# Optimization experiments

Hardware: AMD Instinct MI355X
Metric: run time of the kernel (lower is better)

The kernel has to match this reference:

```python
import jax, jax.numpy as jnp
import numpy as np

B, T, I, H, L = 128, 256, 512, 1024, 2


def setup_inputs() -> dict:
    key = jax.random.key(0)
    ks = jax.random.split(key, 9)
    s_i = 1.0 / np.sqrt(H)
    inp = {
        "x": jax.random.normal(ks[0], (B, T, I), dtype=jnp.float32),
        # layer 0: input_size -> hidden_size
        "W_ih0": jax.random.uniform(ks[1], (4 * H, I), dtype=jnp.float32, minval=-s_i, maxval=s_i),
        "W_hh0": jax.random.uniform(ks[2], (4 * H, H), dtype=jnp.float32, minval=-s_i, maxval=s_i),
        "b_ih0": jax.random.uniform(ks[3], (4 * H,), dtype=jnp.float32, minval=-s_i, maxval=s_i),
        "b_hh0": jax.random.uniform(ks[4], (4 * H,), dtype=jnp.float32, minval=-s_i, maxval=s_i),
        # layer 1: hidden_size -> hidden_size
        "W_ih1": jax.random.uniform(ks[5], (4 * H, H), dtype=jnp.float32, minval=-s_i, maxval=s_i),
        "W_hh1": jax.random.uniform(ks[6], (4 * H, H), dtype=jnp.float32, minval=-s_i, maxval=s_i),
        "b_ih1": jax.random.uniform(ks[7], (4 * H,), dtype=jnp.float32, minval=-s_i, maxval=s_i),
        "b_hh1": jax.random.uniform(ks[8], (4 * H,), dtype=jnp.float32, minval=-s_i, maxval=s_i),
    }
    return inp


def _lstm_cell(xt, h, c, W_ih, W_hh, b_ih, b_hh):
    # gates: [B, 4H] in order i, f, g, o (standard LSTMCell layout)
    gates = xt @ W_ih.T + b_ih + h @ W_hh.T + b_hh
    i, f, g, o = jnp.split(gates, 4, axis=-1)
    c_new = jax.nn.sigmoid(f) * c + jax.nn.sigmoid(i) * jnp.tanh(g)
    h_new = jax.nn.sigmoid(o) * jnp.tanh(c_new)
    return h_new, c_new


def reference(x, W_ih0, W_hh0, b_ih0, b_hh0, W_ih1, W_hh1, b_ih1, b_hh1):
    batch = x.shape[0]
    hidden = W_hh0.shape[1]
    params = ((W_ih0, W_hh0, b_ih0, b_hh0), (W_ih1, W_hh1, b_ih1, b_hh1))
    z = jnp.zeros((batch, hidden), dtype=x.dtype)
    # torch code initializes h and c both from h0 (zeros)
    init = (tuple(z for _ in params), tuple(z for _ in params))

    def step(carry, xt):
        hs, cs = carry
        new_h, new_c = [], []
        layer_in = xt
        for l, (Wi, Wh, bi, bh) in enumerate(params):
            h2, c2 = _lstm_cell(layer_in, hs[l], cs[l], Wi, Wh, bi, bh)
            new_h.append(h2)
            new_c.append(c2)
            layer_in = h2
        return (tuple(new_h), tuple(new_c)), layer_in

    xs = jnp.swapaxes(x, 0, 1)  # [T, B, I]
    _, ys = jax.lax.scan(step, init, xs)
    out = jnp.swapaxes(ys, 0, 1)  # [B, T, H]
    return out
```

## Files before the change

### kernel.cpp

```cpp
#include <hip/hip_runtime.h>

#define B_ 128
#define T_ 256
#define I_ 512
#define H_ 1024

typedef _Float16 f16;
typedef _Float16 v8h __attribute__((ext_vector_type(8)));
typedef _Float16 v2h __attribute__((ext_vector_type(2)));
typedef float v16f __attribute__((ext_vector_type(16)));
typedef int v4i __attribute__((ext_vector_type(4)));

__device__ __forceinline__ float fsigmoid(float x) { return 1.0f / (1.0f + __expf(-x)); }
__device__ __forceinline__ float ftanh(float x) { return 1.0f - 2.0f / (__expf(2.0f * x) + 1.0f); }

__device__ __forceinline__ void gl_lds16(const void* g, void* l) {
    __builtin_amdgcn_global_load_lds(
        (const __attribute__((address_space(1))) unsigned int*)g,
        (__attribute__((address_space(3))) unsigned int*)l, 16, 0, 0);
}
__device__ __forceinline__ void gl_lds16_coh(const void* g, void* l) {
    __builtin_amdgcn_global_load_lds(
        (const __attribute__((address_space(1))) unsigned int*)g,
        (__attribute__((address_space(3))) unsigned int*)l, 16, 0, 17);
}

__device__ __forceinline__ void pollwait(const int* base, int tgt, int lane) {
    if (tgt <= 0) return;
    for (;;) {
        bool ok = true;
        if (lane < 32) {
            v4i v;
            asm volatile("global_load_dwordx4 %0, %1, off sc0 sc1\n\ts_waitcnt vmcnt(0)"
                         : "=&v"(v) : "v"(base + lane * 4) : "memory");
            ok = (v[0] >= tgt) && (v[1] >= tgt) && (v[2] >= tgt) && (v[3] >= tgt);
        }
        if (__ballot(ok) == ~0ULL) return;
        __builtin_amdgcn_s_sleep(1);
    }
}

#define WAITV(n) asm volatile("s_waitcnt vmcnt(" #n ")" ::: "memory")
#define BARX { __builtin_amdgcn_s_barrier(); __builtin_amdgcn_sched_barrier(0); }

__global__ void k_f32_to_f16(const float* __restrict__ in, f16* __restrict__ out, int n) {
    int i = blockIdx.x * blockDim.x + threadIdx.x;
    int st = gridDim.x * blockDim.x;
    for (; i < n; i += st) out[i] = (f16)in[i];
}
__global__ void k_bias_sum(const float* __restrict__ a, const float* __restrict__ b,
                           float* __restrict__ o, int n) {
    int i = blockIdx.x * blockDim.x + threadIdx.x;
    int st = gridDim.x * blockDim.x;
    for (; i < n; i += st) o[i] = a[i] + b[i];
}

template <int SLOT>
__device__ void run_slot8(int mh, int tile, int widx128,
                          const f16* __restrict__ xh,
                          const f16* __restrict__ wi, const f16* __restrict__ wh,
                          const float* __restrict__ bs,
                          f16* __restrict__ h0, f16* __restrict__ h1,
                          float* __restrict__ out, int* flags, char* lds)
{
    constexpr int NKS = SLOT ? 32 : 24;
    const size_t BH = (size_t)B_ * H_;

    const int tid = threadIdx.x;
    const int wave = tid >> 6;
    const int lane = tid & 63;
    const int l31 = lane & 31, khi = lane >> 5;
    const int nw = wave & 1, kw = wave >> 1;
    const int n0 = tile * 16;
    const int rbase = mh * 64;

    const int gcl = nw * 32 + l31;
    const size_t gr = (size_t)(gcl >> 4) * H_ + n0 + (gcl & 15);
    v8h wfrag[NKS];
#pragma unroll
    for (int s = 0; s < NKS; ++s) {
        const f16* p;
        if (SLOT == 0) {
            p = (s < 8) ? (wi + gr * 512 + kw * 128 + s * 16 + khi * 8)
                        : (wh + gr * 1024 + kw * 256 + (s - 8) * 16 + khi * 8);
        } else {
            p = (s < 16) ? (wh + gr * 1024 + kw * 256 + s * 16 + khi * 8)
                         : (wi + gr * 1024 + kw * 256 + (s - 16) * 16 + khi * 8);
        }
        wfrag[s] = *(const v8h*)p;
    }

    const int urow = tid >> 3;
    const int un = (tid & 7) * 2;
    const float2 bI = *(const float2*)(bs + 0 * H_ + n0 + un);
    const float2 bF = *(const float2*)(bs + 1 * H_ + n0 + un);
    const float2 bG = *(const float2*)(bs + 2 * H_ + n0 + un);
    const float2 bO = *(const float2*)(bs + 3 * H_ + n0 + un);
    float c0r = 0.f, c1r = 0.f;

    int* f_own = flags + SLOT * 128;
    int* f_oth = flags + (1 - SLOT) * 128;

    float* gf = (float*)(lds + 49152);

    const int rw_ = lane >> 3;
    const int ss_ = (lane & 7) ^ rw_;

#pragma unroll 1
    for (int p = 0; p <= T_; ++p) {
        const bool active = SLOT ? (p >= 1) : (p < T_);
        const int tau = SLOT ? p - 1 : p;

        const f16* srcA = nullptr; size_t strA = 0; const f16* srcB = nullptr; f16* hout = nullptr;
        if (active) {
            if (SLOT == 0) {
                srcA = xh + (size_t)tau * I_;  strA = (size_t)T_ * I_;
                srcB = h0 + (size_t)((p + 3) & 3) * BH;
                hout = h0 + (size_t)(p & 3) * BH;
            } else {
                srcA = h0 + (size_t)((p + 3) & 3) * BH;
                srcB = h1 + (size_t)((p + 3) & 3) * BH;
                hout = h1 + (size_t)(p & 3) * BH;
            }
        }

        auto issue = [&](int r) {
            const f16* base; size_t str; int koff; bool coh;
            if (SLOT == 0) {
                if (r < 2) { base = srcA; str = strA;      koff = kw * 128 + r * 64;       coh = false; }
                else       { base = srcB; str = (size_t)H_; koff = kw * 256 + (r - 2) * 64; coh = true; }
            } else {
                if (r < 4) { base = srcB; str = (size_t)H_; koff = kw * 256 + r * 64;       coh = true; }
                else       { base = srcA; str = (size_t)H_; koff = kw * 256 + (r - 4) * 64; coh = true; }
            }
            char* dbase = lds + kw * 32768 + (r & 3) * 8192 + nw * 4096;
#pragma unroll
            for (int i = 0; i < 4; ++i) {
                const int rl = rbase + nw * 32 + i * 8 + rw_;
                const f16* gp = base + (size_t)rl * str + koff + ss_ * 8;
                if (coh) gl_lds16_coh(gp, dbase + i * 1024);
                else     gl_lds16(gp, dbase + i * 1024);
            }
        };

        v16f acc0 = {}, acc1 = {};

        auto compute = [&](int r) {
            const char* sb = lds + kw * 32768 + (r & 3) * 8192;
#pragma unroll
            for (int ks = 0; ks < 4; ++ks) {
                const int qo = (((ks * 2 + khi) ^ (l31 & 7)) << 4);
                const v8h a0 = *(const v8h*)(sb + l31 * 128 + qo);
                const v8h a1 = *(const v8h*)(sb + (32 + l31) * 128 + qo);
                __builtin_amdgcn_s_setprio(1);
                acc0 = __builtin_amdgcn_mfma_f32_32x32x16_f16(a0, wfrag[r * 4 + ks], acc0, 0, 0, 0);
                acc1 = __builtin_amdgcn_mfma_f32_32x32x16_f16(a1, wfrag[r * 4 + ks], acc1, 0, 0, 0);
                __builtin_amdgcn_s_setprio(0);
            }
        };

        if (active) {
            if (SLOT == 0) {
                issue(0); issue(1);
                WAITV(4); BARX; compute(0);
                WAITV(0); BARX; compute(1);
                if (wave == 0) pollwait(f_own, p, lane);
                BARX;
                issue(2); issue(3); issue(4);
                WAITV(8); BARX; compute(2); issue(5);
                WAITV(8); BARX; compute(3);
                WAITV(4); BARX; compute(4);
                WAITV(0); BARX; compute(5);
            } else {
                if (wave == 4) pollwait(f_own, p, lane);
                __syncthreads();
                issue(0); issue(1); issue(2);
                WAITV(8); BARX; compute(0); issue(3);
                WAITV(8); BARX; compute(1);
                if (wave == 0) pollwait(f_oth, p, lane);
                BARX;
                issue(4);
                WAITV(8); BARX; compute(2); issue(5);
                WAITV(8); BARX; compute(3); issue(6);
                WAITV(8); BARX; compute(4); issue(7);
                WAITV(8); BARX; compute(5);
                WAITV(4); BARX; compute(6);
                WAITV(0); BARX; compute(7);
            }
            __syncthreads();

            if (kw >= 1) {
                float* rg = (float*)lds + ((kw - 1) * 2 + nw) * 2048;
#pragma unroll
                for (int j = 0; j < 16; ++j) {
                    rg[j * 64 + lane] = acc0[j];
                    rg[(16 + j) * 64 + lane] = acc1[j];
                }
            }
            __syncthreads();
            if (kw == 0) {
                const float* r0 = (float*)lds + (0 + nw) * 2048;
                const float* r1 = (float*)lds + (2 + nw) * 2048;
                const float* r2 = (float*)lds + (4 + nw) * 2048;
#pragma unroll
                for (int j = 0; j < 16; ++j) {
                    const float s0 = acc0[j] + r0[j * 64 + lane] + r1[j * 64 + lane] + r2[j * 64 + lane];
                    const float s1 = acc1[j] + r0[(16 + j) * 64 + lane] + r1[(16 + j) * 64 + lane] + r2[(16 + j) * 64 + lane];
                    const int row = (j & 3) + 8 * (j >> 2) + 4 * khi;
                    gf[row * 68 + nw * 32 + l31] = s0;
                    gf[(32 + row) * 68 + nw * 32 + l31] = s1;
                }
            }
            __syncthreads();

            if (SLOT == 0) {
                if (wave == 0) pollwait(f_oth, p - 2, lane);
                __syncthreads();
            }

            {
                const float* g0 = gf + urow * 68 + un;
                const float xi0 = g0[0] + bI.x,  xi1 = g0[1] + bI.y;
                const float xf0 = g0[16] + bF.x, xf1 = g0[17] + bF.y;
                const float xg0 = g0[32] + bG.x, xg1 = g0[33] + bG.y;
                const float xo0 = g0[48] + bO.x, xo1 = g0[49] + bO.y;
                const float cn0 = fsigmoid(xf0) * c0r + fsigmoid(xi0) * ftanh(xg0);
                const float cn1 = fsigmoid(xf1) * c1r + fsigmoid(xi1) * ftanh(xg1);
                const float hn0 = fsigmoid(xo0) * ftanh(cn0);
                const float hn1 = fsigmoid(xo1) * ftanh(cn1);
                c0r = cn0; c1r = cn1;
                union { v2h h2; unsigned u; } cv;
                cv.h2[0] = (f16)hn0; cv.h2[1] = (f16)hn1;
                unsigned* hp = (unsigned*)(hout + (size_t)(rbase + urow) * H_ + n0 + un);
                asm volatile("global_store_dword %0, %1, off sc0 sc1" :: "v"(hp), "v"(cv.u) : "memory");
                if (SLOT == 1) {
                    float2 yv; yv.x = hn0; yv.y = hn1;
                    *(float2*)(out + ((size_t)(rbase + urow) * T_ + tau) * H_ + n0 + un) = yv;
                }
            }
        }

        asm volatile("s_waitcnt vmcnt(0)" ::: "memory");
        __syncthreads();
        if (tid == 0) {
            int v = p + 1;
            int* fp = f_own + widx128;
            asm volatile("global_store_dword %0, %1, off sc0 sc1" :: "v"(fp), "v"(v) : "memory");
        }
    }
}

__global__ __launch_bounds__(512, 2) void lstm_persist8(
    const f16* __restrict__ xh,
    const f16* __restrict__ w0i, const f16* __restrict__ w0h,
    const f16* __restrict__ w1i, const f16* __restrict__ w1h,
    const float* __restrict__ bs0, const float* __restrict__ bs1,
    f16* __restrict__ h0, f16* __restrict__ h1, float* __restrict__ out,
    int* flags)
{
    __shared__ __align__(16) char lds[131072];
    const int bx = blockIdx.x;
    const int slot = bx & 1;
    const int mh = (bx >> 1) & 1;
    const int tile = bx >> 2;
    const int widx128 = mh * 64 + tile;
    if (slot == 0)
        run_slot8<0>(mh, tile, widx128, xh, w0i, w0h, bs0, h0, h1, out, flags, lds);
    else
        run_slot8<1>(mh, tile, widx128, xh, w1i, w1h, bs1, h0, h1, out, flags, lds);
}

#define BM 64
#define NT 8

__global__ __launch_bounds__(256) void lstm_step(
    const float* __restrict__ A1, long a1_stride, int K1,
    const float* __restrict__ hprev,
    const float* __restrict__ Wih, const float* __restrict__ Whh,
    const float* __restrict__ bih, const float* __restrict__ bhh,
    float* __restrict__ cbuf, float* __restrict__ hout,
    float* yout, long y_stride)
{
    __shared__ float As[32][66];
    __shared__ float Ws[32][36];
    const int tid = threadIdx.x;
    const int n0 = blockIdx.x * NT;
    const int b0 = blockIdx.y * BM;
    const int tb = tid >> 3;
    const int tc = tid & 7;
    const int lr = tid >> 3;
    const int lk = tid & 7;
    const long wj = (long)(lr >> 3) * H_ + n0 + (lr & 7);
    float acc[2][4] = {{0.f, 0.f, 0.f, 0.f}, {0.f, 0.f, 0.f, 0.f}};
#pragma unroll 1
    for (int ph = 0; ph < 2; ++ph) {
        const float* Ap = (ph == 0) ? A1 : hprev;
        const long as = (ph == 0) ? a1_stride : (long)H_;
        const float* W = (ph == 0) ? Wih : Whh;
        const int K = (ph == 0) ? K1 : H_;
        const float* arow0 = Ap + (long)(b0 + lr) * as + 4 * lk;
        const float* arow1 = Ap + (long)(b0 + lr + 32) * as + 4 * lk;
        const float* wrow = W + wj * K + 4 * lk;
        float4 ra0 = *(const float4*)(arow0);
        float4 ra1 = *(const float4*)(arow1);
        float4 rw = *(const float4*)(wrow);
        for (int k0 = 0; k0 < K; k0 += 32) {
            __syncthreads();
            {
                const int kk = 4 * lk;
                As[kk + 0][lr] = ra0.x; As[kk + 1][lr] = ra0.y;
                As[kk + 2][lr] = ra0.z; As[kk + 3][lr] = ra0.w;
                As[kk + 0][lr + 32] = ra1.x; As[kk + 1][lr + 32] = ra1.y;
                As[kk + 2][lr + 32] = ra1.z; As[kk + 3][lr + 32] = ra1.w;
                Ws[kk + 0][lr] = rw.x; Ws[kk + 1][lr] = rw.y;
                Ws[kk + 2][lr] = rw.z; Ws[kk + 3][lr] = rw.w;
            }
            __syncthreads();
            const int kn = k0 + 32;
            if (kn < K) {
                ra0 = *(const float4*)(arow0 + kn);
                ra1 = *(const float4*)(arow1 + kn);
                rw = *(const float4*)(wrow + kn);
            }
#pragma unroll
            for (int k = 0; k < 32; ++k) {
                float2 a = *(const float2*)&As[k][2 * tb];
                float4 w = *(const float4*)&Ws[k][4 * tc];
                acc[0][0] = fmaf(a.x, w.x, acc[0][0]);
                acc[0][1] = fmaf(a.x, w.y, acc[0][1]);
                acc[0][2] = fmaf(a.x, w.z, acc[0][2]);
                acc[0][3] = fmaf(a.x, w.w, acc[0][3]);
                acc[1][0] = fmaf(a.y, w.x, acc[1][0]);
                acc[1][1] = fmaf(a.y, w.y, acc[1][1]);
                acc[1][2] = fmaf(a.y, w.z, acc[1][2]);
                acc[1][3] = fmaf(a.y, w.w, acc[1][3]);
            }
        }
    }
    __syncthreads();
    float* gsf = &As[0][0];
#pragma unroll
    for (int bi = 0; bi < 2; ++bi)
#pragma unroll
        for (int ci = 0; ci < 4; ++ci)
            gsf[(2 * tb + bi) * 33 + 4 * tc + ci] = acc[bi][ci];
    __syncthreads();
    const int dn = tid & 7;
    const int bq = tid >> 3;
    const int n = n0 + dn;
#pragma unroll
    for (int s = 0; s < 2; ++s) {
        const int b = bq + 32 * s;
        float xi = gsf[b * 33 + dn] + bih[n] + bhh[n];
        float xf = gsf[b * 33 + 8 + dn] + bih[H_ + n] + bhh[H_ + n];
        float xg = gsf[b * 33 + 16 + dn] + bih[2 * H_ + n] + bhh[2 * H_ + n];
        float xo = gsf[b * 33 + 24 + dn] + bih[3 * H_ + n] + bhh[3 * H_ + n];
        const long idx = (long)(b0 + b) * H_ + n;
        const float c_old = cbuf[idx];
        const float cn = fsigmoid(xf) * c_old + fsigmoid(xi) * ftanh(xg);
        const float hn = fsigmoid(xo) * ftanh(cn);
        cbuf[idx] = cn;
        hout[idx] = hn;
        if (yout) yout[(long)(b0 + b) * y_stride + n] = hn;
    }
}

extern "C" void kernel_launch(void* const* d_in, const int* in_sizes, int n_in,
                              void* d_out, int out_size, void* d_ws, size_t ws_size,
                              hipStream_t stream) {
    const float* x = (const float*)d_in[0];
    const float* Wih0 = (const float*)d_in[1];
    const float* Whh0 = (const float*)d_in[2];
    const float* bih0 = (const float*)d_in[3];
    const float* bhh0 = (const float*)d_in[4];
    const float* Wih1 = (const float*)d_in[5];
    const float* Whh1 = (const float*)d_in[6];
    const float* bih1 = (const float*)d_in[7];
    const float* bhh1 = (const float*)d_in[8];
    float* out = (float*)d_out;

    const size_t BH = (size_t)B_ * H_;
    const size_t NX = (size_t)B_ * T_ * I_;
    const size_t NW0I = (size_t)4 * H_ * I_;
    const size_t NWH = (size_t)4 * H_ * H_;

    const size_t off_xh = 0;
    const size_t off_w0i = off_xh + NX * 2;
    const size_t off_w0h = off_w0i + NW0I * 2;
    const size_t off_w1i = off_w0h + NWH * 2;
    const size_t off_w1h = off_w1i + NWH * 2;
    const size_t off_bs0 = off_w1h + NWH * 2;
    const size_t off_bs1 = off_bs0 + 4 * H_ * 4;
    const size_t off_h0 = off_bs1 + 4 * H_ * 4;
    const size_t off_h1 = off_h0 + 4 * BH * 2;
    const size_t off_flags = off_h1 + 4 * BH * 2;
    const size_t REQ = off_flags + 256 * 4;

    char* ws = (char*)d_ws;

    if (ws_size >= REQ) {
        f16* xh = (f16*)(ws + off_xh);
        f16* w0i = (f16*)(ws + off_w0i);
        f16* w0h = (f16*)(ws + off_w0h);
        f16* w1i = (f16*)(ws + off_w1i);
        f16* w1h = (f16*)(ws + off_w1h);
        float* bs0 = (float*)(ws + off_bs0);
        float* bs1 = (float*)(ws + off_bs1);
        f16* h0 = (f16*)(ws + off_h0);
        f16* h1 = (f16*)(ws + off_h1);
        int* flags = (int*)(ws + off_flags);

        hipMemsetAsync(ws + off_h0, 0, REQ - off_h0, stream);

        dim3 cb(256);
        k_f32_to_f16<<<2048, cb, 0, stream>>>(x, xh, (int)NX);
        k_f32_to_f16<<<2048, cb, 0, stream>>>(Wih0, w0i, (int)NW0I);
        k_f32_to_f16<<<2048, cb, 0, stream>>>(Whh0, w0h, (int)NWH);
        k_f32_to_f16<<<2048, cb, 0, stream>>>(Wih1, w1i, (int)NWH);
        k_f32_to_f16<<<2048, cb, 0, stream>>>(Whh1, w1h, (int)NWH);
        k_bias_sum<<<16, cb, 0, stream>>>(bih0, bhh0, bs0, 4 * H_);
        k_bias_sum<<<16, cb, 0, stream>>>(bih1, bhh1, bs1, 4 * H_);

        lstm_persist8<<<256, 512, 0, stream>>>(xh, w0i, w0h, w1i, w1h, bs0, bs1,
                                               h0, h1, out, flags);
        return;
    }

    float* fws = (float*)d_ws;
    float* h0a = fws;
    float* h0b = fws + BH;
    float* c0 = fws + 2 * BH;
    float* h1a = fws + 3 * BH;
    float* h1b = fws + 4 * BH;
    float* c1 = fws + 5 * BH;
    hipMemsetAsync(d_ws, 0, 6 * BH * sizeof(float), stream);

    dim3 grid(H_ / NT, B_ / BM);
    dim3 block(256);
    for (int t = 0; t < T_; ++t) {
        float* h0in = (t & 1) ? h0b : h0a;
        float* h0out = (t & 1) ? h0a : h0b;
        float* h1in = (t & 1) ? h1b : h1a;
        float* h1out = (t & 1) ? h1a : h1b;
        lstm_step<<<grid, block, 0, stream>>>(
            x + (size_t)t * I_, (long)T_ * I_, I_,
            h0in, Wih0, Whh0, bih0, bhh0, c0, h0out, nullptr, 0);
        lstm_step<<<grid, block, 0, stream>>>(
            h0out, (long)H_, H_,
            h1in, Wih1, Whh1, bih1, bhh1, c1, h1out,
            out + (size_t)t * H_, (long)T_ * H_);
    }
}
```

Measured before the change: 2.518 ms.

## Split recurrence flags per batch half and unify the K-chunk pipeline

Each block now waits only on the flags of producer blocks covering its own batch half. It polls both needed flag sets (own layer and the other layer) in one combined wait instead of several staggered waits. The K dimension is split evenly across wave groups using a generic loop with a 5-buffer LDS ring and 4-chunk-deep prefetch; LDS grows to 160KB. Layer-0 input chunks are still prefetched before the wait. The layer-1 blocks lose the earlier overlap where part of the GEMM ran before the layer-0 dependency was ready, and the poll sleep interval is longer.

Measured after the change: 2.239 ms. -11.1%, faster.

```diff
diff --git a/kernel.cpp b/kernel.cpp
--- a/kernel.cpp
+++ b/kernel.cpp
@@ -25,18 +25,21 @@
         (__attribute__((address_space(3))) unsigned int*)l, 16, 0, 17);
 }
 
-__device__ __forceinline__ void pollwait(const int* base, int tgt, int lane) {
-    if (tgt <= 0) return;
+__device__ __forceinline__ void pollwait2(const int* baseA, int tA,
+                                          const int* baseB, int tB, int lane) {
+    if (tA <= 0 && tB <= 0) return;
     for (;;) {
         bool ok = true;
         if (lane < 32) {
+            const int* b = (lane < 16) ? baseA : baseB;
+            const int t = (lane < 16) ? tA : tB;
             v4i v;
             asm volatile("global_load_dwordx4 %0, %1, off sc0 sc1\n\ts_waitcnt vmcnt(0)"
-                         : "=&v"(v) : "v"(base + lane * 4) : "memory");
-            ok = (v[0] >= tgt) && (v[1] >= tgt) && (v[2] >= tgt) && (v[3] >= tgt);
+                         : "=&v"(v) : "v"(b + (lane & 15) * 4) : "memory");
+            ok = (t <= 0) || ((v[0] >= t) && (v[1] >= t) && (v[2] >= t) && (v[3] >= t));
         }
         if (__ballot(ok) == ~0ULL) return;
-        __builtin_amdgcn_s_sleep(1);
+        __builtin_amdgcn_s_sleep(4);
     }
 }
 
@@ -56,14 +59,17 @@
 }
 
 template <int SLOT>
-__device__ void run_slot8(int mh, int tile, int widx128,
+__device__ void run_slot9(int mh, int tile,
                           const f16* __restrict__ xh,
                           const f16* __restrict__ wi, const f16* __restrict__ wh,
                           const float* __restrict__ bs,
                           f16* __restrict__ h0, f16* __restrict__ h1,
                           float* __restrict__ out, int* flags, char* lds)
 {
-    constexpr int NKS = SLOT ? 32 : 24;
+    constexpr int K0 = SLOT ? 1024 : 512;
+    constexpr int KW = SLOT ? 512 : 384;
+    constexpr int NR = KW / 64;
+    constexpr int NKS = KW / 16;
     const size_t BH = (size_t)B_ * H_;
 
     const int tid = threadIdx.x;
@@ -79,14 +85,8 @@
     v8h wfrag[NKS];
 #pragma unroll
     for (int s = 0; s < NKS; ++s) {
-        const f16* p;
-        if (SLOT == 0) {
-            p = (s < 8) ? (wi + gr * 512 + kw * 128 + s * 16 + khi * 8)
-                        : (wh + gr * 1024 + kw * 256 + (s - 8) * 16 + khi * 8);
-        } else {
-            p = (s < 16) ? (wh + gr * 1024 + kw * 256 + s * 16 + khi * 8)
-                         : (wi + gr * 1024 + kw * 256 + (s - 16) * 16 + khi * 8);
-        }
+        const int k = kw * KW + s * 16 + khi * 8;
+        const f16* p = (k < K0) ? (wi + gr * K0 + k) : (wh + gr * H_ + (k - K0));
         wfrag[s] = *(const v8h*)p;
     }
 
@@ -98,8 +98,9 @@
     const float2 bO = *(const float2*)(bs + 3 * H_ + n0 + un);
     float c0r = 0.f, c1r = 0.f;
 
-    int* f_own = flags + SLOT * 128;
-    int* f_oth = flags + (1 - SLOT) * 128;
+    int* f_pub = flags + (SLOT * 2 + mh) * 64;
+    const int* fA = flags + mh * 64;
+    const int* fB = flags + (2 + mh) * 64;
 
     float* gf = (float*)(lds + 49152);
 
@@ -118,22 +119,18 @@
                 srcB = h0 + (size_t)((p + 3) & 3) * BH;
                 hout = h0 + (size_t)(p & 3) * BH;
             } else {
-                srcA = h0 + (size_t)((p + 3) & 3) * BH;
+                srcA = h0 + (size_t)((p + 3) & 3) * BH;  strA = H_;
                 srcB = h1 + (size_t)((p + 3) & 3) * BH;
                 hout = h1 + (size_t)(p & 3) * BH;
             }
         }
 
         auto issue = [&](int r) {
+            const int kc = kw * KW + r * 64;
             const f16* base; size_t str; int koff; bool coh;
-            if (SLOT == 0) {
-                if (r < 2) { base = srcA; str = strA;      koff = kw * 128 + r * 64;       coh = false; }
-                else       { base = srcB; str = (size_t)H_; koff = kw * 256 + (r - 2) * 64; coh = true; }
-            } else {
-                if (r < 4) { base = srcB; str = (size_t)H_; koff = kw * 256 + r * 64;       coh = true; }
-                else       { base = srcA; str = (size_t)H_; koff = kw * 256 + (r - 4) * 64; coh = true; }
-            }
-            char* dbase = lds + kw * 32768 + (r & 3) * 8192 + nw * 4096;
+            if (kc < K0) { base = srcA; str = strA; koff = kc; coh = (SLOT == 1); }
+            else         { base = srcB; str = (size_t)H_; koff = kc - K0; coh = true; }
+            char* dbase = lds + kw * 40960 + (r % 5) * 8192 + nw * 4096;
 #pragma unroll
             for (int i = 0; i < 4; ++i) {
                 const int rl = rbase + nw * 32 + i * 8 + rw_;
@@ -146,7 +143,7 @@
         v16f acc0 = {}, acc1 = {};
 
         auto compute = [&](int r) {
-            const char* sb = lds + kw * 32768 + (r & 3) * 8192;
+            const char* sb = lds + kw * 40960 + (r % 5) * 8192;
 #pragma unroll
             for (int ks = 0; ks < 4; ++ks) {
                 const int qo = (((ks * 2 + khi) ^ (l31 & 7)) << 4);
@@ -160,32 +157,30 @@
         };
 
         if (active) {
+            unsigned premask = 0;
             if (SLOT == 0) {
-                issue(0); issue(1);
-                WAITV(4); BARX; compute(0);
-                WAITV(0); BARX; compute(1);
-                if (wave == 0) pollwait(f_own, p, lane);
+#pragma unroll
+                for (int r = 0; r < 4; ++r)
+                    if (kw * KW + r * 64 + 64 <= K0) { issue(r); premask |= 1u << r; }
+            }
+
+            if (wave == 0) pollwait2(fA, p, fB, SLOT ? p : p - 2, lane);
+            __syncthreads();
+            __builtin_amdgcn_sched_barrier(0);
+
+#pragma unroll
+            for (int r = 0; r < 4; ++r)
+                if (!(premask & (1u << r))) issue(r);
+
+#pragma unroll
+            for (int r = 0; r < NR; ++r) {
+                if (r + 4 <= NR)      WAITV(12);
+                else if (r + 3 == NR) WAITV(8);
+                else if (r + 2 == NR) WAITV(4);
+                else                  WAITV(0);
                 BARX;
-                issue(2); issue(3); issue(4);
-                WAITV(8); BARX; compute(2); issue(5);
-                WAITV(8); BARX; compute(3);
-                WAITV(4); BARX; compute(4);
-                WAITV(0); BARX; compute(5);
-            } else {
-                if (wave == 4) pollwait(f_own, p, lane);
-                __syncthreads();
-                issue(0); issue(1); issue(2);
-                WAITV(8); BARX; compute(0); issue(3);
-                WAITV(8); BARX; compute(1);
-                if (wave == 0) pollwait(f_oth, p, lane);
-                BARX;
-                issue(4);
-                WAITV(8); BARX; compute(2); issue(5);
-                WAITV(8); BARX; compute(3); issue(6);
-                WAITV(8); BARX; compute(4); issue(7);
-                WAITV(8); BARX; compute(5);
-                WAITV(4); BARX; compute(6);
-                WAITV(0); BARX; compute(7);
+                if (r + 4 < NR) issue(r + 4);
+                compute(r);
             }
             __syncthreads();
 
@@ -212,11 +207,6 @@
                 }
             }
             __syncthreads();
-
-            if (SLOT == 0) {
-                if (wave == 0) pollwait(f_oth, p - 2, lane);
-                __syncthreads();
-            }
 
             {
                 const float* g0 = gf + urow * 68 + un;
@@ -244,13 +234,13 @@
         __syncthreads();
         if (tid == 0) {
             int v = p + 1;
-            int* fp = f_own + widx128;
+            int* fp = f_pub + tile;
             asm volatile("global_store_dword %0, %1, off sc0 sc1" :: "v"(fp), "v"(v) : "memory");
         }
     }
 }
 
-__global__ __launch_bounds__(512, 2) void lstm_persist8(
+__global__ __launch_bounds__(512, 2) void lstm_persist9(
     const f16* __restrict__ xh,
     const f16* __restrict__ w0i, const f16* __restrict__ w0h,
     const f16* __restrict__ w1i, const f16* __restrict__ w1h,
@@ -258,16 +248,15 @@
     f16* __restrict__ h0, f16* __restrict__ h1, float* __restrict__ out,
     int* flags)
 {
-    __shared__ __align__(16) char lds[131072];
+    __shared__ __align__(16) char lds[163840];
     const int bx = blockIdx.x;
     const int slot = bx & 1;
     const int mh = (bx >> 1) & 1;
     const int tile = bx >> 2;
-    const int widx128 = mh * 64 + tile;
     if (slot == 0)
-        run_slot8<0>(mh, tile, widx128, xh, w0i, w0h, bs0, h0, h1, out, flags, lds);
+        run_slot9<0>(mh, tile, xh, w0i, w0h, bs0, h0, h1, out, flags, lds);
     else
-        run_slot8<1>(mh, tile, widx128, xh, w1i, w1h, bs1, h0, h1, out, flags, lds);
+        run_slot9<1>(mh, tile, xh, w1i, w1h, bs1, h0, h1, out, flags, lds);
 }
 
 #define BM 64
@@ -421,7 +410,7 @@
         k_bias_sum<<<16, cb, 0, stream>>>(bih0, bhh0, bs0, 4 * H_);
         k_bias_sum<<<16, cb, 0, stream>>>(bih1, bhh1, bs1, 4 * H_);
 
-        lstm_persist8<<<256, 512, 0, stream>>>(xh, w0i, w0h, w1i, w1h, bs0, bs1,
+        lstm_persist9<<<256, 512, 0, stream>>>(xh, w0i, w0h, w1i, w1h, bs0, bs1,
                                                h0, h1, out, flags);
         return;
     }
```
